# Performance work log

Hardware: AMD Instinct MI355X
Metric: run time of the kernel (lower is better)

The kernel has to match this reference:

```python
import jax, jax.numpy as jnp
import numpy as np
import math

D_MODEL = 1024
N_HEADS = 16
D_K = D_MODEL // N_HEADS
NB_FEATURES = max(1, math.ceil(math.log(D_MODEL)))  # 7
D_FF = 4096
BH = 4  # block_size_h
BW = 4  # block_size_w
EPS_LN = 1e-6


def gelu_approx(x):
    c = math.sqrt(2.0 / math.pi)
    return 0.5 * x * (1.0 + jnp.tanh(c * (x + 0.044715 * x * x * x)))


def layer_norm(x, alpha, bias):
    # torch .std() uses ddof=1 (unbiased)
    mean = x.mean(axis=-1, keepdims=True)
    std = jnp.std(x, axis=-1, ddof=1, keepdims=True)
    return alpha * (x - mean) / (std + EPS_LN) + bias


def causal_performer(q_in, k_in, v_in, wq, wk, wv, wo, omega):
    B, Sq, D = q_in.shape
    Sk = k_in.shape[1]
    q = (q_in @ wq.T).reshape(B, Sq, N_HEADS, D_K)
    k = (k_in @ wk.T).reshape(B, Sk, N_HEADS, D_K)
    v = (v_in @ wv.T).reshape(B, Sk, N_HEADS, D_K)
    # exp kernel feature map: exp(-0.5 * (x @ omega^T)^2)
    qp = jnp.exp(-0.5 * jnp.square(q @ omega.T))  # (B,Sq,H,nb)
    kp = jnp.exp(-0.5 * jnp.square(k @ omega.T))  # (B,Sk,H,nb)
    qp = qp / (qp.sum(-1, keepdims=True) + 1e-6)
    kp = kp / (kp.sum(-1, keepdims=True) + 1e-6)
    K_cum = jnp.cumsum(kp, axis=1)                               # (B,Sk,H,nb)
    KV_cum = jnp.cumsum(kp[..., None] * v[..., None, :], axis=1)  # (B,Sk,H,nb,dk)
    key_idx = jnp.clip((jnp.arange(Sq) // BH + 1) * BW - 1, None, Sk - 1)
    K_sel = K_cum[:, key_idx]    # (B,Sq,H,nb)
    KV_sel = KV_cum[:, key_idx]  # (B,Sq,H,nb,dk)
    num = jnp.einsum('bshn,bshnd->bshd', qp, KV_sel)
    den = jnp.einsum('bshn,bshn->bsh', qp, K_sel)[..., None]
    out = (num / (den + 1e-6)).reshape(B, Sq, D)
    return out @ wo.T


def setup_inputs() -> dict:
    key = jax.random.key(0)
    ks = jax.random.split(key, 24)
    s = 0.02
    p = {}
    p['x'] = jax.random.normal(ks[0], (2, 4096, D_MODEL), jnp.float32)
    p['lto'] = jax.random.normal(ks[1], (2, 4096, D_MODEL), jnp.float32)
    for i, nm in enumerate(['wq_s', 'wk_s', 'wv_s', 'wo_s']):
        p[nm] = jax.random.normal(ks[2 + i], (D_MODEL, D_MODEL), jnp.float32) * s
    for i, nm in enumerate(['wq_c', 'wk_c', 'wv_c', 'wo_c']):
        p[nm] = jax.random.normal(ks[6 + i], (D_MODEL, D_MODEL), jnp.float32) * s
    p['omega_s'] = jax.random.normal(ks[10], (NB_FEATURES, D_K), jnp.float32) / math.sqrt(D_K)
    p['omega_c'] = jax.random.normal(ks[11], (NB_FEATURES, D_K), jnp.float32) / math.sqrt(D_K)
    p['w1'] = jax.random.normal(ks[12], (D_FF, D_MODEL), jnp.float32) * s
    p['b1'] = jnp.zeros((D_FF,), jnp.float32)
    p['w2'] = jax.random.normal(ks[13], (D_MODEL, D_FF), jnp.float32) * s
    p['b2'] = jnp.zeros((D_MODEL,), jnp.float32)
    for i in range(3):
        p[f'ln{i}_a'] = jnp.ones((D_MODEL,), jnp.float32)
        p[f'ln{i}_b'] = jnp.zeros((D_MODEL,), jnp.float32)
    return p


def reference(x, lto, wq_s, wk_s, wv_s, wo_s, wq_c, wk_c, wv_c, wo_c,
              omega_s, omega_c, w1, b1, w2, b2,
              ln0_a, ln0_b, ln1_a, ln1_b, ln2_a, ln2_b):
    # residual 0: self-attention on x
    xn = layer_norm(x, ln0_a, ln0_b)
    x = x + causal_performer(xn, xn, xn, wq_s, wk_s, wv_s, wo_s, omega_s)
    # residual 1: cross-attention, queries = normed lto, keys/values = updated x
    ln = layer_norm(lto, ln1_a, ln1_b)
    lto = lto + causal_performer(ln, x, x, wq_c, wk_c, wv_c, wo_c, omega_c)
    # residual 2: feed-forward
    fn = layer_norm(lto, ln2_a, ln2_b)
    ff = gelu_approx(fn @ w1.T + b1) @ w2.T + b2
    return lto + ff
```

## Files before the change

### kernel.cpp

```cpp
#include <hip/hip_runtime.h>
#include <cstdint>
#include <cstddef>

typedef __bf16 bf16;
typedef __bf16 bf16x8 __attribute__((ext_vector_type(8)));
typedef __bf16 bf16x4 __attribute__((ext_vector_type(4)));
typedef float  f32x4  __attribute__((ext_vector_type(4)));

#define NB 7
static constexpr int Bq = 2, Sq = 4096, Dm = 1024, Dff = 4096;
static constexpr int Mrows = Bq * Sq;
static constexpr int NCH = Sq / 4;
static constexpr int CSW = 464;

__device__ __forceinline__ void gload16(const void* g, void* l) {
  __builtin_amdgcn_global_load_lds((__attribute__((address_space(1))) void*)g,
                                   (__attribute__((address_space(3))) void*)l,
                                   16, 0, 0);
}

template <int N> __device__ __forceinline__ void wait_vmcnt() {
  asm volatile("s_waitcnt vmcnt(%0)" :: "n"(N) : "memory");
}
__device__ __forceinline__ void wait_lgkm0() {
  asm volatile("s_waitcnt lgkmcnt(0)" ::: "memory");
}
__device__ __forceinline__ void sbar() {
  __builtin_amdgcn_sched_barrier(0);
  __builtin_amdgcn_s_barrier();
  __builtin_amdgcn_sched_barrier(0);
}

__device__ __forceinline__ float gelu_f(float x) {
  const float c = 0.79788456080286535588f;
  float z = c * (x + 0.044715f * x * x * x);
  float t = 1.f - 2.f / (__expf(2.f * z) + 1.f);
  return 0.5f * x * (1.f + t);
}

struct CvtA {
  const float* s[10];
  bf16* d[10];
  int start[11];
};
__global__ __launch_bounds__(256) void cvt10(CvtA a) {
  const int i = blockIdx.x * 256 + threadIdx.x;
  int r = 0;
#pragma unroll
  for (int k = 1; k < 10; ++k) r += (i >= a.start[k]);
  const int o = i - a.start[r];
  f32x4 v = *(const f32x4*)&a.s[r][(size_t)o * 4];
  bf16x4 ov;
#pragma unroll
  for (int e = 0; e < 4; ++e) ov[e] = (bf16)v[e];
  *(bf16x4*)&a.d[r][(size_t)o * 4] = ov;
}

__global__ __launch_bounds__(256) void ln_kernel(const float* __restrict__ x,
                                                 const float* __restrict__ alpha,
                                                 const float* __restrict__ beta,
                                                 bf16* __restrict__ out) {
  const int row = blockIdx.x, tid = threadIdx.x;
  const float* xr = x + (size_t)row * Dm;
  f32x4 v = *(const f32x4*)&xr[tid * 4];
  float s  = v[0] + v[1] + v[2] + v[3];
  float s2 = v[0]*v[0] + v[1]*v[1] + v[2]*v[2] + v[3]*v[3];
#pragma unroll
  for (int o = 32; o > 0; o >>= 1) { s += __shfl_xor(s, o); s2 += __shfl_xor(s2, o); }
  __shared__ float red[8];
  const int wid = tid >> 6, lane = tid & 63;
  if (lane == 0) { red[wid] = s; red[wid + 4] = s2; }
  __syncthreads();
  s  = red[0] + red[1] + red[2] + red[3];
  s2 = red[4] + red[5] + red[6] + red[7];
  const float mean = s * (1.f / 1024.f);
  float var = (s2 - s * mean) * (1.f / 1023.f);
  var = fmaxf(var, 0.f);
  const float inv = 1.f / (sqrtf(var) + 1e-6f);
  f32x4 a4 = *(const f32x4*)&alpha[tid * 4];
  f32x4 b4 = *(const f32x4*)&beta[tid * 4];
  bf16x4 o4;
#pragma unroll
  for (int e = 0; e < 4; ++e) o4[e] = (bf16)(a4[e] * (v[e] - mean) * inv + b4[e]);
  *(bf16x4*)&out[(size_t)row * Dm + tid * 4] = o4;
}

template <int MODE>
__global__ __launch_bounds__(512, 2) void gemm256(
    const bf16* __restrict__ A, const bf16* __restrict__ Bw,
    int M, int N, int K,
    const float* __restrict__ bias, bf16* __restrict__ outB) {
  __shared__ __align__(16) bf16 As[2][256 * 64];
  __shared__ __align__(16) bf16 Bs[2][256 * 64];

  const int tid = threadIdx.x;
  const int lane = tid & 63, wid = tid >> 6;
  const int wm = wid >> 2, wn = wid & 3;

  int bid = blockIdx.x;
  const int nwg = gridDim.x;
  bid = (bid & 7) * (nwg >> 3) + (bid >> 3);
  const int nbx = N >> 8;
  const int bm = (bid / nbx) * 256, bn = (bid % nbx) * 256;
  const int NT = K >> 6, NI = NT >> 1;

  const int srow = tid >> 3;
  const int scol = ((tid & 7) ^ (srow & 7)) * 8;
  const bf16* Ag = A  + (size_t)(bm + srow) * K + scol;
  const bf16* Bg = Bw + (size_t)(bn + srow) * K + scol;

  auto stA = [&](int buf, int H, int t) {
#pragma unroll
    for (int c = 0; c < 2; ++c)
      gload16(Ag + (size_t)(H * 128 + c * 64) * K + (size_t)t * 64,
              (char*)(&As[buf][0]) + H * 16384 + c * 8192 + wid * 1024);
  };
  auto stB = [&](int buf, int H, int t) {
#pragma unroll
    for (int c = 0; c < 2; ++c)
      gload16(Bg + (size_t)(H * 128 + c * 64) * K + (size_t)t * 64,
              (char*)(&Bs[buf][0]) + H * 16384 + c * 8192 + wid * 1024);
  };

  f32x4 acc[8][4] = {};
  const int lr = lane & 15, uo = lane >> 4;

  auto ldA = [&](const bf16* Asb, int mh, bf16x8 (&a)[4][2]) {
#pragma unroll
    for (int i = 0; i < 4; ++i)
#pragma unroll
      for (int kh = 0; kh < 2; ++kh) {
        const int r = wm * 128 + mh * 64 + i * 16 + lr;
        const int u = (kh * 4 + uo) ^ (lr & 7);
        a[i][kh] = *(const bf16x8*)&Asb[r * 64 + u * 8];
      }
  };
  auto ldB = [&](const bf16* Bsb, int nh, bf16x8 (&b)[2][2]) {
#pragma unroll
    for (int j = 0; j < 2; ++j)
#pragma unroll
      for (int kh = 0; kh < 2; ++kh) {
        const int r = wn * 64 + nh * 32 + j * 16 + lr;
        const int u = (kh * 4 + uo) ^ (lr & 7);
        b[j][kh] = *(const bf16x8*)&Bsb[r * 64 + u * 8];
      }
  };
  auto mm = [&](int mh, int nh, bf16x8 (&a)[4][2], bf16x8 (&b)[2][2]) {
    __builtin_amdgcn_s_setprio(1);
#pragma unroll
    for (int i = 0; i < 4; ++i)
#pragma unroll
      for (int j = 0; j < 2; ++j) {
        acc[mh*4+i][nh*2+j] = __builtin_amdgcn_mfma_f32_16x16x32_bf16(
            a[i][0], b[j][0], acc[mh*4+i][nh*2+j], 0, 0, 0);
        acc[mh*4+i][nh*2+j] = __builtin_amdgcn_mfma_f32_16x16x32_bf16(
            a[i][1], b[j][1], acc[mh*4+i][nh*2+j], 0, 0, 0);
      }
    __builtin_amdgcn_s_setprio(0);
  };

  stB(0, 0, 0); stB(0, 1, 0); stA(0, 0, 0); stA(0, 1, 0);
  stB(1, 0, 1); stA(1, 0, 1);
  wait_vmcnt<4>();
  __builtin_amdgcn_s_barrier();

  for (int t = 0; t < NI; ++t) {
    const int u = 2 * t;
    const bool more = (t + 1 < NI);
#pragma unroll
    for (int hf = 0; hf < 2; ++hf) {
      const bf16* Asb = &As[hf][0];
      const bf16* Bsb = &Bs[hf][0];
      bf16x8 a[4][2], b0[2][2], b1[2][2];

      ldA(Asb, 0, a); ldB(Bsb, 0, b0);
      __builtin_amdgcn_sched_barrier(0);
      if (hf == 0) stB(1, 1, u + 1);
      else if (more) stB(0, 1, u + 2);
      sbar();
      wait_lgkm0();
      __builtin_amdgcn_sched_barrier(0);
      mm(0, 0, a, b0);
      sbar();

      ldB(Bsb, 1, b1);
      __builtin_amdgcn_sched_barrier(0);
      if (hf == 0) stA(1, 1, u + 1);
      else if (more) stA(0, 1, u + 2);
      sbar();
      wait_lgkm0();
      __builtin_amdgcn_sched_barrier(0);
      mm(0, 1, a, b1);
      sbar();

      ldA(Asb, 1, a);
      __builtin_amdgcn_sched_barrier(0);
      if (more) { if (hf == 0) stB(0, 0, u + 2); else stB(1, 0, u + 3); }
      sbar();
      wait_lgkm0();
      __builtin_amdgcn_sched_barrier(0);
      mm(1, 1, a, b1);
      sbar();

      if (more) { if (hf == 0) stA(0, 0, u + 2); else stA(1, 0, u + 3); }
      __builtin_amdgcn_sched_barrier(0);
      sbar();
      mm(1, 0, a, b0);
      __builtin_amdgcn_sched_barrier(0);
      if (hf == 0) { if (more) wait_vmcnt<4>(); else wait_vmcnt<0>(); }
      else if (more) wait_vmcnt<4>();
      __builtin_amdgcn_s_barrier();
      __builtin_amdgcn_sched_barrier(0);
    }
  }

#pragma unroll
  for (int f = 0; f < 8; ++f) {
    const int r0 = bm + wm * 128 + f * 16 + (lane >> 4) * 4;
#pragma unroll
    for (int g = 0; g < 4; ++g) {
      const int c = bn + wn * 64 + g * 16 + (lane & 15);
      float bv = 0.f;
      if (MODE == 3) bv = bias[c];
#pragma unroll
      for (int r = 0; r < 4; ++r) {
        const size_t idx = (size_t)(r0 + r) * N + c;
        float v = acc[f][g][r];
        if (MODE == 3) v = gelu_f(v + bv);
        outB[idx] = (bf16)v;
      }
    }
  }
}

template <int MODE>
__global__ __launch_bounds__(256, 2) void gemm128(
    const bf16* __restrict__ A, const bf16* __restrict__ Bw,
    int M, int N, int K,
    const float* __restrict__ bias, const float* __restrict__ res,
    float* __restrict__ outF, bf16* __restrict__ outB) {
  constexpr int BM = 128, BN = 128;
  __shared__ __align__(16) bf16 As[2][BM * 64];
  __shared__ __align__(16) bf16 Bs[2][BN * 64];

  const int tid = threadIdx.x;
  const int lane = tid & 63, wid = tid >> 6;
  const int wm = wid >> 1, wn = wid & 1;

  int bid = blockIdx.x;
  const int nwg = gridDim.x;
  bid = (bid & 7) * (nwg >> 3) + (bid >> 3);
  const int nbx = N / BN;
  const int bm = (bid / nbx) * BM, bn = (bid % nbx) * BN;
  const int NT = K >> 6;

  const int srow = tid >> 3;
  const int scol = ((tid & 7) ^ (srow & 7)) * 8;
  const bf16* Ag = A  + (size_t)(bm + srow) * K + scol;
  const bf16* Bg = Bw + (size_t)(bn + srow) * K + scol;

  f32x4 acc[4][4] = {};
  const int lr = lane & 15, uo = lane >> 4;

  auto stA = [&](int buf, int t) {
#pragma unroll
    for (int c = 0; c < 4; ++c)
      gload16(Ag + ((size_t)(c * 32) * K + (size_t)t * 64),
              (char*)(&As[buf][0]) + c * 4096 + wid * 1024);
  };
  auto stB = [&](int buf, int t) {
#pragma unroll
    for (int c = 0; c < 4; ++c)
      gload16(Bg + ((size_t)(c * 32) * K + (size_t)t * 64),
              (char*)(&Bs[buf][0]) + c * 4096 + wid * 1024);
  };

  stA(0, 0); stB(0, 0);
  stA(1, 1); stB(1, 1);
  wait_vmcnt<8>();
  __builtin_amdgcn_s_barrier();

  bf16x8 a[4][2], b[4][2];

  for (int t = 0; t < NT; ++t) {
    const int cur = t & 1;
    const bf16* Asb = &As[cur][0];
    const bf16* Bsb = &Bs[cur][0];

#pragma unroll
    for (int i = 0; i < 4; ++i)
#pragma unroll
      for (int kh = 0; kh < 2; ++kh) {
        const int r = wm * 64 + i * 16 + lr;
        const int u = (kh * 4 + uo) ^ (lr & 7);
        a[i][kh] = *(const bf16x8*)&Asb[r * 64 + u * 8];
      }
#pragma unroll
    for (int j = 0; j < 4; ++j)
#pragma unroll
      for (int kh = 0; kh < 2; ++kh) {
        const int r = wn * 64 + j * 16 + lr;
        const int u = (kh * 4 + uo) ^ (lr & 7);
        b[j][kh] = *(const bf16x8*)&Bsb[r * 64 + u * 8];
      }
    wait_lgkm0();
    __builtin_amdgcn_sched_barrier(0);
    __builtin_amdgcn_s_barrier();
    __builtin_amdgcn_sched_barrier(0);

    if (t + 2 < NT) { stA(cur, t + 2); stB(cur, t + 2); }
    __builtin_amdgcn_sched_barrier(0);

    __builtin_amdgcn_s_setprio(1);
#pragma unroll
    for (int i = 0; i < 4; ++i)
#pragma unroll
      for (int j = 0; j < 4; ++j) {
        acc[i][j] = __builtin_amdgcn_mfma_f32_16x16x32_bf16(a[i][0], b[j][0], acc[i][j], 0, 0, 0);
        acc[i][j] = __builtin_amdgcn_mfma_f32_16x16x32_bf16(a[i][1], b[j][1], acc[i][j], 0, 0, 0);
      }
    __builtin_amdgcn_s_setprio(0);
    __builtin_amdgcn_sched_barrier(0);

    if (t < NT - 2) wait_vmcnt<8>();
    else            wait_vmcnt<0>();
    __builtin_amdgcn_s_barrier();
    __builtin_amdgcn_sched_barrier(0);
  }

#pragma unroll
  for (int f = 0; f < 4; ++f) {
    const int r0 = bm + wm * 64 + f * 16 + (lane >> 4) * 4;
#pragma unroll
    for (int g = 0; g < 4; ++g) {
      const int c = bn + wn * 64 + g * 16 + (lane & 15);
      float bv = 0.f;
      if (MODE == 3 || MODE == 4) bv = bias[c];
#pragma unroll
      for (int r = 0; r < 4; ++r) {
        const size_t idx = (size_t)(r0 + r) * N + c;
        float v = acc[f][g][r];
        if (MODE == 1 || MODE == 2) v += res[idx];
        if (MODE == 3) v = gelu_f(v + bv);
        if (MODE == 4) v += bv + res[idx];
        if (MODE == 0 || MODE == 1 || MODE == 3) outB[idx] = (bf16)v;
        else outF[idx] = v;
      }
    }
  }
}

__global__ __launch_bounds__(512) void perf_cs(
    const bf16* __restrict__ kmat, const bf16* __restrict__ vmat, int ld,
    const float* __restrict__ omega, float* __restrict__ CS,
    float* __restrict__ segtot) {
  const int tid = threadIdx.x;
  const int bh = blockIdx.y, b = bh >> 4, h = bh & 15;
  const int seg = blockIdx.x;
  const int s0 = seg * 512;
  __shared__ __align__(16) bf16 vs[512][64];
  __shared__ float kps[512][8];
  __shared__ float oms[448];

  {
    const bf16* vb = vmat + ((size_t)(b * Sq + s0)) * ld + h * 64;
#pragma unroll
    for (int p = 0; p < 8; ++p) {
      const int row = p * 64 + (tid >> 3), c16 = (tid & 7) * 8;
      *(uint4*)&vs[row][c16 ^ ((row & 7) * 8)] =
          *(const uint4*)&vb[(size_t)row * ld + c16];
    }
  }
  if (tid < 448) oms[tid] = omega[tid];
  __syncthreads();

  {
    const int row = tid;
    const bf16* kr = kmat + ((size_t)(b * Sq + s0 + row)) * ld + h * 64;
    bf16x8 kv[8];
#pragma unroll
    for (int q = 0; q < 8; ++q) kv[q] = *(const bf16x8*)&kr[q * 8];
    float f[NB];
#pragma unroll
    for (int n = 0; n < NB; ++n) f[n] = 0.f;
#pragma unroll
    for (int d = 0; d < 64; ++d) {
      const float kd = (float)kv[d >> 3][d & 7];
#pragma unroll
      for (int n = 0; n < NB; ++n) f[n] += kd * oms[n * 64 + d];
    }
    float sum = 1e-6f, e[NB];
#pragma unroll
    for (int n = 0; n < NB; ++n) { e[n] = __expf(-0.5f * f[n] * f[n]); sum += e[n]; }
    const float inv = 1.f / sum;
#pragma unroll
    for (int n = 0; n < NB; ++n) kps[row][n] = e[n] * inv;
    kps[row][7] = 0.f;
  }
  __syncthreads();

  if (tid < CSW) {
    const int comp = tid;
    float* outb = CS + ((size_t)bh * NCH + seg * 128) * CSW;
    float r = 0.f;
    if (comp < 8) {
      for (int c = 0; c < 128; ++c) {
        if (comp < 7)
          r += kps[4*c][comp] + kps[4*c+1][comp] + kps[4*c+2][comp] + kps[4*c+3][comp];
        outb[(size_t)c * CSW + comp] = r;
      }
    } else if (comp < 456) {
      const int n = (comp - 8) >> 6, d = (comp - 8) & 63;
      for (int c = 0; c < 128; ++c) {
#pragma unroll
        for (int i = 0; i < 4; ++i) {
          const int row = 4 * c + i;
          r += kps[row][n] * (float)vs[row][d ^ ((row & 7) * 8)];
        }
        outb[(size_t)c * CSW + comp] = r;
      }
    } else {
      for (int c = 0; c < 128; ++c) outb[(size_t)c * CSW + comp] = 0.f;
    }
    segtot[((size_t)bh * 8 + seg) * CSW + comp] = r;
  }
}

__global__ __launch_bounds__(256) void perf_scan2(float* __restrict__ segtot) {
  const int bh = blockIdx.x;
  const int c0 = threadIdx.x;
  float run0 = 0.f, run1 = 0.f;
#pragma unroll
  for (int s = 0; s < 8; ++s) {
    float* st = segtot + ((size_t)bh * 8 + s) * CSW;
    float t0 = st[c0]; st[c0] = run0; run0 += t0;
    if (c0 + 256 < CSW) { float t1 = st[c0 + 256]; st[c0 + 256] = run1; run1 += t1; }
  }
}

__global__ __launch_bounds__(256) void perf_out(
    const bf16* __restrict__ qmat, int ldq, const float* __restrict__ omega,
    const float* __restrict__ CS, const float* __restrict__ segtot,
    bf16* __restrict__ attn) {
  const int tid = threadIdx.x;
  const int bh = blockIdx.y, b = bh >> 4, h = bh & 15;
  const int s0 = blockIdx.x * 128;
  const int cg0 = s0 >> 2;
  const int seg = cg0 >> 7;
  __shared__ __align__(16) float Ps[32 * CSW];
  __shared__ float qps[128][8];
  __shared__ float oms[NB * 64];

  {
    const float* src = CS + ((size_t)bh * NCH + cg0) * CSW;
    const float* off = segtot + ((size_t)bh * 8 + seg) * CSW;
    for (int i = tid; i < 32 * CSW / 4; i += 256) {
      f32x4 a = *(const f32x4*)&src[i * 4];
      f32x4 o = *(const f32x4*)&off[(i % (CSW / 4)) * 4];
      a += o;
      *(f32x4*)&Ps[i * 4] = a;
    }
  }
  if (tid < 224) { oms[tid] = omega[tid]; oms[tid + 224] = omega[tid + 224]; }
  __syncthreads();
  {
    const int p = tid >> 1, half = tid & 1;
    const bf16* qr = qmat + ((size_t)(b * Sq + s0 + p)) * ldq + h * 64 + half * 32;
    bf16x8 qv[4];
#pragma unroll
    for (int q = 0; q < 4; ++q) qv[q] = *(const bf16x8*)&qr[q * 8];
    float f[NB];
#pragma unroll
    for (int n = 0; n < NB; ++n) f[n] = 0.f;
#pragma unroll
    for (int d = 0; d < 32; ++d) {
      float qd = (float)qv[d >> 3][d & 7];
#pragma unroll
      for (int n = 0; n < NB; ++n) f[n] += qd * oms[n * 64 + half * 32 + d];
    }
    float sum = 1e-6f;
    float e[NB];
#pragma unroll
    for (int n = 0; n < NB; ++n) {
      float full = f[n] + __shfl_xor(f[n], 1);
      e[n] = __expf(-0.5f * full * full);
      sum += e[n];
    }
    float inv = 1.f / sum;
    if (half == 0) {
      float den = 1e-6f;
      const float* Pr = &Ps[(p >> 2) * CSW];
#pragma unroll
      for (int n = 0; n < NB; ++n) {
        float qn = e[n] * inv;
        qps[p][n] = qn;
        den += qn * Pr[n];
      }
      qps[p][7] = 1.f / den;
    }
  }
  __syncthreads();
  {
    const int d = tid & 63, w = tid >> 6;
    for (int qq = w; qq < 128; qq += 4) {
      const float* Pr = &Ps[(qq >> 2) * CSW + 8 + d];
      float num = 0.f;
#pragma unroll
      for (int n = 0; n < NB; ++n) num += qps[qq][n] * Pr[n * 64];
      attn[((size_t)(b * Sq + s0 + qq)) * Dm + h * 64 + d] = (bf16)(num * qps[qq][7]);
    }
  }
}

extern "C" void kernel_launch(void* const* d_in, const int* in_sizes, int n_in,
                              void* d_out, int out_size, void* d_ws, size_t ws_size,
                              hipStream_t stream) {
  const float* x    = (const float*)d_in[0];
  const float* lto  = (const float*)d_in[1];
  const float* w_s[4] = {(const float*)d_in[2], (const float*)d_in[3],
                         (const float*)d_in[4], (const float*)d_in[5]};
  const float* w_c[4] = {(const float*)d_in[6], (const float*)d_in[7],
                         (const float*)d_in[8], (const float*)d_in[9]};
  const float* omega_s = (const float*)d_in[10];
  const float* omega_c = (const float*)d_in[11];
  const float* w1 = (const float*)d_in[12];
  const float* b1 = (const float*)d_in[13];
  const float* w2 = (const float*)d_in[14];
  const float* b2 = (const float*)d_in[15];
  const float* ln_a[3] = {(const float*)d_in[16], (const float*)d_in[18], (const float*)d_in[20]};
  const float* ln_b[3] = {(const float*)d_in[17], (const float*)d_in[19], (const float*)d_in[21]};

  char* ws = (char*)d_ws;
  size_t off = 0;
  auto alloc = [&](size_t bytes) -> char* {
    char* p = ws + off;
    off += (bytes + 255) & ~(size_t)255;
    return p;
  };

  const size_t actB = (size_t)Mrows * Dm * sizeof(bf16);
  const size_t MB32 = (size_t)Mrows * 2048 * sizeof(bf16);

  bf16* wqkv = (bf16*)alloc((size_t)3072 * 1024 * 2);
  bf16* wo_sb = (bf16*)alloc((size_t)1024 * 1024 * 2);
  bf16* wq_cb = (bf16*)alloc((size_t)1024 * 1024 * 2);
  bf16* wkv  = (bf16*)alloc((size_t)2048 * 1024 * 2);
  bf16* wo_cb = (bf16*)alloc((size_t)1024 * 1024 * 2);
  bf16* w1b = (bf16*)alloc((size_t)Dff * Dm * 2);
  bf16* w2b = (bf16*)alloc((size_t)Dff * Dm * 2);
  bf16* xnb  = (bf16*)alloc(actB);
  char* pool = alloc((size_t)Mrows * Dff * 2);
  bf16* qkvb = (bf16*)pool;
  bf16* kvb  = (bf16*)pool;
  bf16* qb   = (bf16*)(pool + MB32);
  bf16* hb   = (bf16*)pool;
  bf16* attnb= (bf16*)alloc(actB);
  bf16* x2b  = (bf16*)alloc(actB);
  bf16* ln1b = (bf16*)alloc(actB);
  float* lto2 = (float*)alloc((size_t)Mrows * Dm * 4);
  float* CSb  = (float*)alloc((size_t)32 * NCH * CSW * 4);
  float* stb  = (float*)alloc((size_t)32 * 8 * CSW * 4);
  bf16* fnb = xnb;

  {
    CvtA a;
    const float* srcs[10] = {w_s[0], w_s[1], w_s[2], w_s[3], w_c[0],
                             w_c[1], w_c[2], w_c[3], w1, w2};
    bf16* dsts[10] = {wqkv, wqkv + 1048576, wqkv + 2097152, wo_sb, wq_cb,
                      wkv, wkv + 1048576, wo_cb, w1b, w2b};
    const int SM = 262144, LG = 1048576;
    int st = 0;
    for (int i = 0; i < 10; ++i) {
      a.s[i] = srcs[i]; a.d[i] = dsts[i]; a.start[i] = st;
      st += (i < 8) ? SM : LG;
    }
    a.start[10] = st;
    cvt10<<<st / 256, 256, 0, stream>>>(a);
  }

  dim3 gperf(Sq / 128, Bq * 16);
  dim3 gseg(8, Bq * 16);
  const int gQKV = (Mrows / 256) * (3072 / 256);
  const int gKV  = (Mrows / 256) * (2048 / 256);
  const int gFF1 = (Mrows / 256) * (4096 / 256);
  const int gN1k = (Mrows / 128) * (1024 / 128);

  ln_kernel<<<Mrows, 256, 0, stream>>>(x, ln_a[0], ln_b[0], xnb);
  gemm256<0><<<gQKV, 512, 0, stream>>>(xnb, wqkv, Mrows, 3072, 1024, nullptr, qkvb);
  perf_cs<<<gseg, 512, 0, stream>>>(qkvb + 1024, qkvb + 2048, 3072, omega_s, CSb, stb);
  perf_scan2<<<32, 256, 0, stream>>>(stb);
  perf_out<<<gperf, 256, 0, stream>>>(qkvb, 3072, omega_s, CSb, stb, attnb);
  gemm128<1><<<gN1k, 256, 0, stream>>>(attnb, wo_sb, Mrows, 1024, 1024, nullptr, x, nullptr, x2b);

  ln_kernel<<<Mrows, 256, 0, stream>>>(lto, ln_a[1], ln_b[1], ln1b);
  gemm128<0><<<gN1k, 256, 0, stream>>>(ln1b, wq_cb, Mrows, 1024, 1024, nullptr, nullptr, nullptr, qb);
  gemm256<0><<<gKV, 512, 0, stream>>>(x2b, wkv, Mrows, 2048, 1024, nullptr, kvb);
  perf_cs<<<gseg, 512, 0, stream>>>(kvb, kvb + 1024, 2048, omega_c, CSb, stb);
  perf_scan2<<<32, 256, 0, stream>>>(stb);
  perf_out<<<gperf, 256, 0, stream>>>(qb, 1024, omega_c, CSb, stb, attnb);
  gemm128<2><<<gN1k, 256, 0, stream>>>(attnb, wo_cb, Mrows, 1024, 1024, nullptr, lto, lto2, nullptr);

  ln_kernel<<<Mrows, 256, 0, stream>>>(lto2, ln_a[2], ln_b[2], fnb);
  gemm256<3><<<gFF1, 512, 0, stream>>>(fnb, w1b, Mrows, 4096, 1024, b1, hb);
  gemm128<4><<<gN1k, 256, 0, stream>>>(hb, w2b, Mrows, 1024, 4096, b2, lto2, (float*)d_out, nullptr);
}
```

Baseline: 531.9 us.

## Prefetch MFMA fragments across barriers and split-K FFN2 onto the 256-tile GEMM

The 256x256 GEMM main loop is reordered so the next quarter's LDS fragments load into separate register sets while the current MFMAs run. The old pattern of barrier, then a full lgkm wait before every MFMA batch is removed, and the vmcnt waits are relaxed. The second FFN GEMM (K=4096) moves from the 128x128 kernel to the 256x256 kernel with a 2-way split-K, which writes bf16 partial sums. A new elementwise kernel then adds the two partials, the bias and the residual. This trades more register pressure and an extra reduction pass for better MFMA utilisation. Rounding the partials to bf16 adds precision loss, and the partial buffer reuses attnb, so it relies on the allocation after it being free.

```diff
diff --git a/kernel.cpp b/kernel.cpp
--- a/kernel.cpp
+++ b/kernel.cpp
@@ -25,11 +25,7 @@
 __device__ __forceinline__ void wait_lgkm0() {
   asm volatile("s_waitcnt lgkmcnt(0)" ::: "memory");
 }
-__device__ __forceinline__ void sbar() {
-  __builtin_amdgcn_sched_barrier(0);
-  __builtin_amdgcn_s_barrier();
-  __builtin_amdgcn_sched_barrier(0);
-}
+__device__ __forceinline__ void SB() { __builtin_amdgcn_sched_barrier(0); }
 
 __device__ __forceinline__ float gelu_f(float x) {
   const float c = 0.79788456080286535588f;
@@ -85,9 +81,9 @@
   *(bf16x4*)&out[(size_t)row * Dm + tid * 4] = o4;
 }
 
-template <int MODE>
+template <int MODE, int SK>
 __global__ __launch_bounds__(512, 2) void gemm256(
-    const bf16* __restrict__ A, const bf16* __restrict__ Bw,
+    const bf16* __restrict__ A, int lda, const bf16* __restrict__ Bw, int ldb,
     int M, int N, int K,
     const float* __restrict__ bias, bf16* __restrict__ outB) {
   __shared__ __align__(16) bf16 As[2][256 * 64];
@@ -96,6 +92,13 @@
   const int tid = threadIdx.x;
   const int lane = tid & 63, wid = tid >> 6;
   const int wm = wid >> 2, wn = wid & 3;
+
+  if (SK) {
+    const int ks = blockIdx.y;
+    A    += (size_t)ks * K;
+    Bw   += (size_t)ks * K;
+    outB += (size_t)ks * M * N;
+  }
 
   int bid = blockIdx.x;
   const int nwg = gridDim.x;
@@ -106,24 +109,26 @@
 
   const int srow = tid >> 3;
   const int scol = ((tid & 7) ^ (srow & 7)) * 8;
-  const bf16* Ag = A  + (size_t)(bm + srow) * K + scol;
-  const bf16* Bg = Bw + (size_t)(bn + srow) * K + scol;
+  const bf16* Ag = A  + (size_t)(bm + srow) * lda + scol;
+  const bf16* Bg = Bw + (size_t)(bn + srow) * ldb + scol;
 
   auto stA = [&](int buf, int H, int t) {
 #pragma unroll
     for (int c = 0; c < 2; ++c)
-      gload16(Ag + (size_t)(H * 128 + c * 64) * K + (size_t)t * 64,
+      gload16(Ag + (size_t)(H * 128 + c * 64) * lda + (size_t)t * 64,
               (char*)(&As[buf][0]) + H * 16384 + c * 8192 + wid * 1024);
   };
   auto stB = [&](int buf, int H, int t) {
 #pragma unroll
     for (int c = 0; c < 2; ++c)
-      gload16(Bg + (size_t)(H * 128 + c * 64) * K + (size_t)t * 64,
+      gload16(Bg + (size_t)(H * 128 + c * 64) * ldb + (size_t)t * 64,
               (char*)(&Bs[buf][0]) + H * 16384 + c * 8192 + wid * 1024);
   };
 
   f32x4 acc[8][4] = {};
   const int lr = lane & 15, uo = lane >> 4;
+
+  bf16x8 A0[4][2], A1[4][2], B0[2][2], B1[2][2];
 
   auto ldA = [&](const bf16* Asb, int mh, bf16x8 (&a)[4][2]) {
 #pragma unroll
@@ -145,7 +150,7 @@
         b[j][kh] = *(const bf16x8*)&Bsb[r * 64 + u * 8];
       }
   };
-  auto mm = [&](int mh, int nh, bf16x8 (&a)[4][2], bf16x8 (&b)[2][2]) {
+  auto mmq = [&](int mh, int nh, bf16x8 (&a)[4][2], bf16x8 (&b)[2][2]) {
     __builtin_amdgcn_s_setprio(1);
 #pragma unroll
     for (int i = 0; i < 4; ++i)
@@ -163,6 +168,8 @@
   stB(1, 0, 1); stA(1, 0, 1);
   wait_vmcnt<4>();
   __builtin_amdgcn_s_barrier();
+  ldA(&As[0][0], 0, A0); ldB(&Bs[0][0], 0, B0);
+  SB();
 
   for (int t = 0; t < NI; ++t) {
     const int u = 2 * t;
@@ -171,46 +178,37 @@
     for (int hf = 0; hf < 2; ++hf) {
       const bf16* Asb = &As[hf][0];
       const bf16* Bsb = &Bs[hf][0];
-      bf16x8 a[4][2], b0[2][2], b1[2][2];
-
-      ldA(Asb, 0, a); ldB(Bsb, 0, b0);
-      __builtin_amdgcn_sched_barrier(0);
+
+      wait_lgkm0(); SB();
+      ldB(Bsb, 1, B1); SB();
+      mmq(0, 0, A0, B0); SB();
       if (hf == 0) stB(1, 1, u + 1);
       else if (more) stB(0, 1, u + 2);
-      sbar();
-      wait_lgkm0();
-      __builtin_amdgcn_sched_barrier(0);
-      mm(0, 0, a, b0);
-      sbar();
-
-      ldB(Bsb, 1, b1);
-      __builtin_amdgcn_sched_barrier(0);
+      SB(); __builtin_amdgcn_s_barrier(); SB();
+
+      wait_lgkm0(); SB();
+      ldA(Asb, 1, A1); SB();
+      mmq(0, 1, A0, B1); SB();
       if (hf == 0) stA(1, 1, u + 1);
       else if (more) stA(0, 1, u + 2);
-      sbar();
-      wait_lgkm0();
-      __builtin_amdgcn_sched_barrier(0);
-      mm(0, 1, a, b1);
-      sbar();
-
-      ldA(Asb, 1, a);
-      __builtin_amdgcn_sched_barrier(0);
+      SB(); __builtin_amdgcn_s_barrier(); SB();
+
+      wait_lgkm0(); SB();
+      mmq(1, 0, A1, B0); SB();
       if (more) { if (hf == 0) stB(0, 0, u + 2); else stB(1, 0, u + 3); }
-      sbar();
-      wait_lgkm0();
-      __builtin_amdgcn_sched_barrier(0);
-      mm(1, 1, a, b1);
-      sbar();
-
+      SB(); __builtin_amdgcn_s_barrier(); SB();
+
+      if (!(hf == 1 && !more)) {
+        if (hf == 0 && !more) wait_vmcnt<0>();
+        else                  wait_vmcnt<2>();
+        SB();
+        ldA(&As[hf ^ 1][0], 0, A0);
+        ldB(&Bs[hf ^ 1][0], 0, B0);
+      }
+      SB();
+      mmq(1, 1, A1, B1); SB();
       if (more) { if (hf == 0) stA(0, 0, u + 2); else stA(1, 0, u + 3); }
-      __builtin_amdgcn_sched_barrier(0);
-      sbar();
-      mm(1, 0, a, b0);
-      __builtin_amdgcn_sched_barrier(0);
-      if (hf == 0) { if (more) wait_vmcnt<4>(); else wait_vmcnt<0>(); }
-      else if (more) wait_vmcnt<4>();
-      __builtin_amdgcn_s_barrier();
-      __builtin_amdgcn_sched_barrier(0);
+      SB(); __builtin_amdgcn_s_barrier(); SB();
     }
   }
 
@@ -233,11 +231,31 @@
   }
 }
 
+__global__ __launch_bounds__(256) void ffn2red(
+    const bf16* __restrict__ p0, const bf16* __restrict__ p1,
+    const float* __restrict__ bias, const float* __restrict__ res,
+    float* __restrict__ out) {
+  const size_t i = ((size_t)blockIdx.x * 256 + threadIdx.x) * 8;
+  bf16x8 a = *(const bf16x8*)&p0[i];
+  bf16x8 b = *(const bf16x8*)&p1[i];
+  f32x4 r0 = *(const f32x4*)&res[i];
+  f32x4 r1 = *(const f32x4*)&res[i + 4];
+  const int c = (int)(i & 1023);
+  f32x4 o0, o1;
+#pragma unroll
+  for (int e = 0; e < 4; ++e) {
+    o0[e] = (float)a[e] + (float)b[e] + bias[c + e] + r0[e];
+    o1[e] = (float)a[4 + e] + (float)b[4 + e] + bias[c + 4 + e] + r1[e];
+  }
+  *(f32x4*)&out[i] = o0;
+  *(f32x4*)&out[i + 4] = o1;
+}
+
 template <int MODE>
 __global__ __launch_bounds__(256, 2) void gemm128(
     const bf16* __restrict__ A, const bf16* __restrict__ Bw,
     int M, int N, int K,
-    const float* __restrict__ bias, const float* __restrict__ res,
+    const float* __restrict__ res,
     float* __restrict__ outF, bf16* __restrict__ outB) {
   constexpr int BM = 128, BN = 128;
   __shared__ __align__(16) bf16 As[2][BM * 64];
@@ -304,12 +322,12 @@
         b[j][kh] = *(const bf16x8*)&Bsb[r * 64 + u * 8];
       }
     wait_lgkm0();
-    __builtin_amdgcn_sched_barrier(0);
+    SB();
     __builtin_amdgcn_s_barrier();
-    __builtin_amdgcn_sched_barrier(0);
+    SB();
 
     if (t + 2 < NT) { stA(cur, t + 2); stB(cur, t + 2); }
-    __builtin_amdgcn_sched_barrier(0);
+    SB();
 
     __builtin_amdgcn_s_setprio(1);
 #pragma unroll
@@ -320,12 +338,12 @@
         acc[i][j] = __builtin_amdgcn_mfma_f32_16x16x32_bf16(a[i][1], b[j][1], acc[i][j], 0, 0, 0);
       }
     __builtin_amdgcn_s_setprio(0);
-    __builtin_amdgcn_sched_barrier(0);
+    SB();
 
     if (t < NT - 2) wait_vmcnt<8>();
     else            wait_vmcnt<0>();
     __builtin_amdgcn_s_barrier();
-    __builtin_amdgcn_sched_barrier(0);
+    SB();
   }
 
 #pragma unroll
@@ -334,16 +352,12 @@
 #pragma unroll
     for (int g = 0; g < 4; ++g) {
       const int c = bn + wn * 64 + g * 16 + (lane & 15);
-      float bv = 0.f;
-      if (MODE == 3 || MODE == 4) bv = bias[c];
 #pragma unroll
       for (int r = 0; r < 4; ++r) {
         const size_t idx = (size_t)(r0 + r) * N + c;
         float v = acc[f][g][r];
         if (MODE == 1 || MODE == 2) v += res[idx];
-        if (MODE == 3) v = gelu_f(v + bv);
-        if (MODE == 4) v += bv + res[idx];
-        if (MODE == 0 || MODE == 1 || MODE == 3) outB[idx] = (bf16)v;
+        if (MODE == 0 || MODE == 1) outB[idx] = (bf16)v;
         else outF[idx] = v;
       }
     }
@@ -561,6 +575,7 @@
   float* CSb  = (float*)alloc((size_t)32 * NCH * CSW * 4);
   float* stb  = (float*)alloc((size_t)32 * 8 * CSW * 4);
   bf16* fnb = xnb;
+  bf16* ppb = attnb;
 
   {
     CvtA a;
@@ -586,21 +601,22 @@
   const int gN1k = (Mrows / 128) * (1024 / 128);
 
   ln_kernel<<<Mrows, 256, 0, stream>>>(x, ln_a[0], ln_b[0], xnb);
-  gemm256<0><<<gQKV, 512, 0, stream>>>(xnb, wqkv, Mrows, 3072, 1024, nullptr, qkvb);
+  gemm256<0, 0><<<gQKV, 512, 0, stream>>>(xnb, 1024, wqkv, 1024, Mrows, 3072, 1024, nullptr, qkvb);
   perf_cs<<<gseg, 512, 0, stream>>>(qkvb + 1024, qkvb + 2048, 3072, omega_s, CSb, stb);
   perf_scan2<<<32, 256, 0, stream>>>(stb);
   perf_out<<<gperf, 256, 0, stream>>>(qkvb, 3072, omega_s, CSb, stb, attnb);
-  gemm128<1><<<gN1k, 256, 0, stream>>>(attnb, wo_sb, Mrows, 1024, 1024, nullptr, x, nullptr, x2b);
+  gemm128<1><<<gN1k, 256, 0, stream>>>(attnb, wo_sb, Mrows, 1024, 1024, x, nullptr, x2b);
 
   ln_kernel<<<Mrows, 256, 0, stream>>>(lto, ln_a[1], ln_b[1], ln1b);
-  gemm128<0><<<gN1k, 256, 0, stream>>>(ln1b, wq_cb, Mrows, 1024, 1024, nullptr, nullptr, nullptr, qb);
-  gemm256<0><<<gKV, 512, 0, stream>>>(x2b, wkv, Mrows, 2048, 1024, nullptr, kvb);
+  gemm128<0><<<gN1k, 256, 0, stream>>>(ln1b, wq_cb, Mrows, 1024, 1024, nullptr, nullptr, qb);
+  gemm256<0, 0><<<gKV, 512, 0, stream>>>(x2b, 1024, wkv, 1024, Mrows, 2048, 1024, nullptr, kvb);
   perf_cs<<<gseg, 512, 0, stream>>>(kvb, kvb + 1024, 2048, omega_c, CSb, stb);
   perf_scan2<<<32, 256, 0, stream>>>(stb);
   perf_out<<<gperf, 256, 0, stream>>>(qb, 1024, omega_c, CSb, stb, attnb);
-  gemm128<2><<<gN1k, 256, 0, stream>>>(attnb, wo_cb, Mrows, 1024, 1024, nullptr, lto, lto2, nullptr);
+  gemm128<2><<<gN1k, 256, 0, stream>>>(attnb, wo_cb, Mrows, 1024, 1024, lto, lto2, nullptr);
 
   ln_kernel<<<Mrows, 256, 0, stream>>>(lto2, ln_a[2], ln_b[2], fnb);
-  gemm256<3><<<gFF1, 512, 0, stream>>>(fnb, w1b, Mrows, 4096, 1024, b1, hb);
-  gemm128<4><<<gN1k, 256, 0, stream>>>(hb, w2b, Mrows, 1024, 4096, b2, lto2, (float*)d_out, nullptr);
-}
+  gemm256<3, 0><<<gFF1, 512, 0, stream>>>(fnb, 1024, w1b, 1024, Mrows, 4096, 1024, b1, hb);
+  gemm256<0, 1><<<dim3(128, 2), 512, 0, stream>>>(hb, 4096, w2b, 4096, Mrows, 1024, 2048, nullptr, ppb);
+  ffn2red<<<Mrows * 1024 / 8 / 256, 256, 0, stream>>>(ppb, ppb + (size_t)Mrows * 1024, b2, lto2, (float*)d_out);
+}
```

New measurement: 826.8 us. +55.4%, slower.
